# Optimization experiments

Hardware: AMD Instinct MI355X
Metric: run time of the kernel (lower is better)

## Reference

```python
import jax, jax.numpy as jnp
import numpy as np

B, S, D_MODEL, D_FORWARD, HEAD = 4, 2048, 1024, 1024, 16
D_K = D_FORWARD // HEAD


def setup_inputs() -> dict:
    key = jax.random.key(0)
    ks = jax.random.split(key, 6)
    scale = 1.0 / np.sqrt(D_MODEL)
    x = jax.random.normal(ks[0], (B, S, D_MODEL), dtype=jnp.float32)
    # per-head projection weights, PyTorch Linear layout [out, in] stacked over heads
    Wq = jax.random.normal(ks[1], (HEAD, D_K, D_MODEL), dtype=jnp.float32) * scale
    Wk = jax.random.normal(ks[2], (HEAD, D_K, D_MODEL), dtype=jnp.float32) * scale
    Wv = jax.random.normal(ks[3], (HEAD, D_K, D_MODEL), dtype=jnp.float32) * scale
    Wo = jax.random.normal(ks[4], (D_MODEL, D_FORWARD), dtype=jnp.float32) * (1.0 / np.sqrt(D_FORWARD))
    bo = jax.random.normal(ks[5], (D_MODEL,), dtype=jnp.float32) * 0.01
    return {"x": x, "Wq": Wq, "Wk": Wk, "Wv": Wv, "Wo": Wo, "bo": bo}


def reference(x, Wq, Wk, Wv, Wo, bo):
    d_k = Wq.shape[1]
    # fused per-head projections: q,k,v are [B, H, S, d_k]
    q = jnp.einsum("bsm,hkm->bhsk", x, Wq)
    k = jnp.einsum("bsm,hkm->bhsk", x, Wk)
    v = jnp.einsum("bsm,hkm->bhsk", x, Wv)
    # raw scores [B, H, S, S]
    scores = jnp.einsum("bhqd,bhkd->bhqk", q, k)
    # custom zero-value mask: entries that are exactly 0 get -1e9
    scores = jnp.where(scores != 0, scores, jnp.float32(-1e9))
    # NOTE: original divides by scale_factor = d_k**-0.5, i.e. multiplies by sqrt(d_k)
    att = jax.nn.softmax(scores * jnp.sqrt(jnp.float32(d_k)), axis=-1)
    z = jnp.einsum("bhqk,bhkd->bhqd", att, v)  # [B, H, S, d_k]
    n_batch, h, s, _ = z.shape
    z = jnp.transpose(z, (0, 2, 1, 3)).reshape(n_batch, s, h * d_k)  # [B, S, d_forward]
    return z @ Wo.T + bo
```

## Files before the change

kernel.cpp:

```cpp
#include <hip/hip_runtime.h>
#include <stdint.h>

typedef __attribute__((ext_vector_type(4))) float f32x4;
typedef __attribute__((ext_vector_type(8))) _Float16 half8;
typedef __attribute__((ext_vector_type(4))) unsigned int u32x4;
typedef __attribute__((ext_vector_type(2))) unsigned int u32x2;

#define MFMA_F16(a, b, c) __builtin_amdgcn_mfma_f32_16x16x32_f16(a, b, c, 0, 0, 0)

#define GLD16(gp, lp)                                                          \
  __builtin_amdgcn_global_load_lds(                                            \
      (const __attribute__((address_space(1))) void*)(gp),                     \
      (__attribute__((address_space(3))) void*)(lp), 16, 0, 0)

__device__ __forceinline__ short f2h(float f) {
  union { _Float16 h; short s; } v;
  v.h = (_Float16)f;
  return v.s;
}
__device__ __forceinline__ float exp2_hw(float x) {
  float r;
  asm("v_exp_f32 %0, %1" : "=v"(r) : "v"(x));
  return r;
}
__device__ __forceinline__ uint32_t pkhf(float lo, float hi) {
  uint32_t r;
  asm("v_cvt_pkrtz_f16_f32 %0, %1, %2" : "=v"(r) : "v"(lo), "v"(hi));
  return r;
}

__global__ __launch_bounds__(256) void cast4_f16(const float* __restrict__ src,
                                                 short* __restrict__ d, int n4) {
  int i = blockIdx.x * 256 + threadIdx.x;
  if (i < n4) {
    f32x4 v = *reinterpret_cast<const f32x4*>(src + (size_t)i * 4);
    u32x2 o;
    o[0] = pkhf(v[0], v[1]);
    o[1] = pkhf(v[2], v[3]);
    *reinterpret_cast<u32x2*>(d + (size_t)i * 4) = o;
  }
}

__global__ __launch_bounds__(256) void gemm_proj(
    const short* __restrict__ Xf, const short* __restrict__ Wf,
    short* __restrict__ Qf, short* __restrict__ Kf, short* __restrict__ Vt) {
  __shared__ short sA[128 * 32], sB[128 * 32];
  const int tid = threadIdx.x, lane = tid & 63, w = tid >> 6;
  const int wr = w >> 1, wc = w & 1;
  const int g = lane >> 4, c = lane & 15;
  const int m0 = blockIdx.y * 128, n0 = blockIdx.x * 128;

  f32x4 acc[4][4];
#pragma unroll
  for (int i = 0; i < 4; i++)
#pragma unroll
    for (int j = 0; j < 4; j++) acc[i][j] = (f32x4){0.f, 0.f, 0.f, 0.f};

  const int swG = (g ^ ((c >> 1) & 3)) * 8;

  for (int ks = 0; ks < 32; ks++) {
    const int k0 = ks * 32;
    __syncthreads();
#pragma unroll
    for (int i = 0; i < 2; i++) {
      const int chunk = i * 256 + w * 64 + lane;
      const int row = chunk >> 2;
      const int colg = (chunk & 3) ^ ((row >> 1) & 3);
      const size_t aoff = (size_t)(m0 + row) * 1024 + k0 + colg * 8;
      const size_t boff = (size_t)(n0 + row) * 1024 + k0 + colg * 8;
      const int ldsoff = chunk * 16;
      GLD16(Xf + aoff, (char*)sA + ldsoff);
      GLD16(Wf + boff, (char*)sB + ldsoff);
    }
    asm volatile("s_waitcnt vmcnt(0)" ::: "memory");
    __syncthreads();

    half8 a[4], b8[4];
#pragma unroll
    for (int i = 0; i < 4; i++) {
      a[i] = *(const half8*)&sA[(wr * 64 + i * 16 + c) * 32 + swG];
      b8[i] = *(const half8*)&sB[(wc * 64 + i * 16 + c) * 32 + swG];
    }
#pragma unroll
    for (int i = 0; i < 4; i++)
#pragma unroll
      for (int j = 0; j < 4; j++) acc[i][j] = MFMA_F16(a[i], b8[j], acc[i][j]);
  }

  const int section = n0 >> 10;
#pragma unroll
  for (int i = 0; i < 4; i++)
#pragma unroll
    for (int j = 0; j < 4; j++)
#pragma unroll
      for (int r = 0; r < 4; r++) {
        const float v = acc[i][j][r];
        const int m = m0 + wr * 64 + i * 16 + g * 4 + r;
        const int n = n0 + wc * 64 + j * 16 + c;
        const int b = m >> 11, s = m & 2047;
        const int nn = n & 1023;
        const int hh = nn >> 6, d = nn & 63;
        if (section == 0) {
          const size_t off = ((size_t)(b * 16 + hh) * 2048 + s) * 64 + d;
          Qf[off] = f2h(v * 11.5415603271f);
        } else if (section == 1) {
          const size_t off = ((size_t)(b * 16 + hh) * 2048 + s) * 64 + d;
          Kf[off] = f2h(v);
        } else {
          Vt[((size_t)(b * 16 + hh) * 64 + d) * 2048 + s] = f2h(v);
        }
      }
}

__global__ __launch_bounds__(256) void attn_kernel(
    const short* __restrict__ Qf, const short* __restrict__ Kf,
    const short* __restrict__ Vt, short* __restrict__ Z) {
  __shared__ short sK[2][64 * 64];
  __shared__ short sV[2][64 * 64];
  const int tid = threadIdx.x, lane = tid & 63, w = tid >> 6;
  const int g = lane >> 4, c = lane & 15;
  const int L = blockIdx.x;
  const int wid = (L & 7) * 256 + (L >> 3);
  const int qblk = wid & 31, bh = wid >> 5;
  const int b = bh >> 4, h = bh & 15;
  const size_t base = (size_t)bh * (2048 * 64);

  half8 qf[2];
  {
    const int qrow = qblk * 64 + w * 16 + c;
#pragma unroll
    for (int cc = 0; cc < 2; cc++) {
      const size_t off = base + (size_t)qrow * 64 + cc * 32 + g * 8;
      qf[cc] = *(const half8*)(Qf + off);
    }
  }

  f32x4 zacc[4];
  float m_run = -INFINITY, l_part = 0.f;
#pragma unroll
  for (int dt = 0; dt < 4; dt++) zacc[dt] = (f32x4){0.f, 0.f, 0.f, 0.f};

  const int sw0 = ((0 * 4 + g) ^ (c & 7)) * 8;
  const int sw1 = ((1 * 4 + g) ^ (c & 7)) * 8;

  const int ch0 = tid, ch1 = tid + 256;
  const int kr0 = ch0 >> 3, kc0 = (ch0 & 7) ^ (kr0 & 7);
  const int kr1 = ch1 >> 3, kc1 = (ch1 & 7) ^ (kr1 & 7);
  const int kofs0 = kr0 * 64 + kc0 * 8, kofs1 = kr1 * 64 + kc1 * 8;
  const int vofs0 = kr0 * 2048 + kc0 * 8, vofs1 = kr1 * 2048 + kc1 * 8;
  const int ldo0 = ch0 * 16, ldo1 = ch1 * 16;

  auto stage = [&](int buf, int kt) {
    const size_t kb = base + (size_t)kt * 4096;
    const size_t vb = base + (size_t)kt * 64;
    GLD16(Kf + kb + kofs0, (char*)&sK[buf][0] + ldo0);
    GLD16(Kf + kb + kofs1, (char*)&sK[buf][0] + ldo1);
    GLD16(Vt + vb + vofs0, (char*)&sV[buf][0] + ldo0);
    GLD16(Vt + vb + vofs1, (char*)&sV[buf][0] + ldo1);
  };

  const int srcl = ((g & 1) << 5) + c;

  auto compute = [&](int buf) {
    f32x4 sacc[4];
#pragma unroll
    for (int t = 0; t < 4; t++) sacc[t] = (f32x4){0.f, 0.f, 0.f, 0.f};
    __builtin_amdgcn_s_setprio(1);
#pragma unroll
    for (int cc = 0; cc < 2; cc++) {
      const int sw = cc ? sw1 : sw0;
#pragma unroll
      for (int t = 0; t < 4; t++) {
        const int kr = (t * 16 + c) * 64 + sw;
        half8 k8 = *(const half8*)&sK[buf][kr];
        sacc[t] = MFMA_F16(k8, qf[cc], sacc[t]);
      }
    }
    __builtin_amdgcn_s_setprio(0);

    float p[16];
#pragma unroll
    for (int t = 0; t < 4; t++)
#pragma unroll
      for (int r = 0; r < 4; r++) p[t * 4 + r] = sacc[t][r];
    float m01 = fmaxf(fmaxf(fmaxf(p[0], p[1]), fmaxf(p[2], p[3])),
                      fmaxf(fmaxf(p[4], p[5]), fmaxf(p[6], p[7])));
    float m23 = fmaxf(fmaxf(fmaxf(p[8], p[9]), fmaxf(p[10], p[11])),
                      fmaxf(fmaxf(p[12], p[13]), fmaxf(p[14], p[15])));
    float mx = fmaxf(m01, m23);
    mx = fmaxf(mx, __shfl_xor(mx, 16));
    mx = fmaxf(mx, __shfl_xor(mx, 32));
    if (__any(mx - m_run > 8.0f)) {
      const float mnew = fmaxf(m_run, mx);
      const float sc = exp2_hw(m_run - mnew);
      m_run = mnew;
      l_part *= sc;
#pragma unroll
      for (int dt = 0; dt < 4; dt++)
#pragma unroll
        for (int r = 0; r < 4; r++) zacc[dt][r] *= sc;
    }
#pragma unroll
    for (int i = 0; i < 16; i++) p[i] = exp2_hw(p[i] - m_run);
    l_part += (((p[0] + p[1]) + (p[2] + p[3])) + ((p[4] + p[5]) + (p[6] + p[7]))) +
              (((p[8] + p[9]) + (p[10] + p[11])) +
               ((p[12] + p[13]) + (p[14] + p[15])));

    union { u32x4 u; half8 s; } pf0, pf1;
    {
      const uint32_t wA0 = pkhf(p[0], p[1]), wA1 = pkhf(p[2], p[3]);
      const uint32_t wB0 = pkhf(p[4], p[5]), wB1 = pkhf(p[6], p[7]);
      const uint32_t a0 = __shfl(wA0, srcl), a1 = __shfl(wA1, srcl);
      const uint32_t b0 = __shfl(wB0, srcl), b1 = __shfl(wB1, srcl);
      const uint32_t a2 = __shfl(wA0, srcl + 16), a3 = __shfl(wA1, srcl + 16);
      const uint32_t b2 = __shfl(wB0, srcl + 16), b3 = __shfl(wB1, srcl + 16);
      pf0.u[0] = (g < 2) ? a0 : b0;
      pf0.u[1] = (g < 2) ? a1 : b1;
      pf0.u[2] = (g < 2) ? a2 : b2;
      pf0.u[3] = (g < 2) ? a3 : b3;
    }
    {
      const uint32_t wA0 = pkhf(p[8], p[9]), wA1 = pkhf(p[10], p[11]);
      const uint32_t wB0 = pkhf(p[12], p[13]), wB1 = pkhf(p[14], p[15]);
      const uint32_t a0 = __shfl(wA0, srcl), a1 = __shfl(wA1, srcl);
      const uint32_t b0 = __shfl(wB0, srcl), b1 = __shfl(wB1, srcl);
      const uint32_t a2 = __shfl(wA0, srcl + 16), a3 = __shfl(wA1, srcl + 16);
      const uint32_t b2 = __shfl(wB0, srcl + 16), b3 = __shfl(wB1, srcl + 16);
      pf1.u[0] = (g < 2) ? a0 : b0;
      pf1.u[1] = (g < 2) ? a1 : b1;
      pf1.u[2] = (g < 2) ? a2 : b2;
      pf1.u[3] = (g < 2) ? a3 : b3;
    }

    __builtin_amdgcn_s_setprio(1);
#pragma unroll
    for (int dt = 0; dt < 4; dt++) {
      const int vr = (dt * 16 + c) * 64;
      half8 vb0 = *(const half8*)&sV[buf][vr + sw0];
      half8 vb1 = *(const half8*)&sV[buf][vr + sw1];
      zacc[dt] = MFMA_F16(vb0, pf0.s, zacc[dt]);
      zacc[dt] = MFMA_F16(vb1, pf1.s, zacc[dt]);
    }
    __builtin_amdgcn_s_setprio(0);
  };

  stage(0, 0);
  asm volatile("s_waitcnt vmcnt(0)" ::: "memory");
  __builtin_amdgcn_s_barrier();

#pragma unroll 1
  for (int t2 = 0; t2 < 16; t2++) {
    {
      stage(1, 2 * t2 + 1);
      compute(0);
      asm volatile("s_waitcnt vmcnt(0) lgkmcnt(0)" ::: "memory");
      __builtin_amdgcn_s_barrier();
    }
    {
      const int nxt = 2 * t2 + 2;
      stage(0, nxt < 32 ? nxt : 31);
      compute(1);
      asm volatile("s_waitcnt vmcnt(0) lgkmcnt(0)" ::: "memory");
      __builtin_amdgcn_s_barrier();
    }
  }

  float rs = l_part;
  rs += __shfl_xor(rs, 16);
  rs += __shfl_xor(rs, 32);
  const float inv = rs > 0.f ? 1.0f / rs : 0.f;
  const int qg = qblk * 64 + w * 16 + c;
#pragma unroll
  for (int dt = 0; dt < 4; dt++) {
    u32x2 zw;
    zw[0] = pkhf(zacc[dt][0] * inv, zacc[dt][1] * inv);
    zw[1] = pkhf(zacc[dt][2] * inv, zacc[dt][3] * inv);
    *reinterpret_cast<u32x2*>(
        &Z[(size_t)(b * 2048 + qg) * 1024 + h * 64 + dt * 16 + g * 4]) = zw;
  }
}

__global__ __launch_bounds__(256) void gemm_out(
    const short* __restrict__ Zb, const short* __restrict__ Wof,
    const float* __restrict__ bo, float* __restrict__ out) {
  __shared__ short sA[128 * 32], sB[128 * 32];
  const int tid = threadIdx.x, lane = tid & 63, w = tid >> 6;
  const int wr = w >> 1, wc = w & 1;
  const int g = lane >> 4, c = lane & 15;
  const int m0 = blockIdx.y * 128, n0 = blockIdx.x * 128;

  f32x4 acc[4][4];
#pragma unroll
  for (int i = 0; i < 4; i++)
#pragma unroll
    for (int j = 0; j < 4; j++) acc[i][j] = (f32x4){0.f, 0.f, 0.f, 0.f};

  const int swG = (g ^ ((c >> 1) & 3)) * 8;

  for (int ks = 0; ks < 32; ks++) {
    const int k0 = ks * 32;
    __syncthreads();
#pragma unroll
    for (int i = 0; i < 2; i++) {
      const int chunk = i * 256 + w * 64 + lane;
      const int row = chunk >> 2;
      const int colg = (chunk & 3) ^ ((row >> 1) & 3);
      const size_t aoff = (size_t)(m0 + row) * 1024 + k0 + colg * 8;
      const size_t boff = (size_t)(n0 + row) * 1024 + k0 + colg * 8;
      const int ldsoff = chunk * 16;
      GLD16(Zb + aoff, (char*)sA + ldsoff);
      GLD16(Wof + boff, (char*)sB + ldsoff);
    }
    asm volatile("s_waitcnt vmcnt(0)" ::: "memory");
    __syncthreads();

    half8 a[4], b8[4];
#pragma unroll
    for (int i = 0; i < 4; i++) {
      a[i] = *(const half8*)&sA[(wr * 64 + i * 16 + c) * 32 + swG];
      b8[i] = *(const half8*)&sB[(wc * 64 + i * 16 + c) * 32 + swG];
    }
#pragma unroll
    for (int i = 0; i < 4; i++)
#pragma unroll
      for (int j = 0; j < 4; j++) acc[i][j] = MFMA_F16(a[i], b8[j], acc[i][j]);
  }

#pragma unroll
  for (int i = 0; i < 4; i++)
#pragma unroll
    for (int j = 0; j < 4; j++)
#pragma unroll
      for (int r = 0; r < 4; r++) {
        const int m = m0 + wr * 64 + i * 16 + g * 4 + r;
        const int n = n0 + wc * 64 + j * 16 + c;
        out[(size_t)m * 1024 + n] = acc[i][j][r] + bo[n];
      }
}

extern "C" void kernel_launch(void* const* d_in, const int* in_sizes, int n_in,
                              void* d_out, int out_size, void* d_ws, size_t ws_size,
                              hipStream_t stream) {
  const float* x  = (const float*)d_in[0];
  const float* Wq = (const float*)d_in[1];
  const float* Wk = (const float*)d_in[2];
  const float* Wv = (const float*)d_in[3];
  const float* Wo = (const float*)d_in[4];
  const float* bo = (const float*)d_in[5];
  float* out = (float*)d_out;

  const size_t NX = 8388608;
  const size_t NW = 1048576;
  const size_t NQ = 8388608;

  char* p = (char*)d_ws;
  auto take = [&](size_t bytes) -> char* {
    char* r = p;
    p += (bytes + 255) & ~(size_t)255;
    return r;
  };
  short* Xf  = (short*)take(NX * 2);
  short* Wf  = (short*)take(3 * NW * 2);
  short* Wof = (short*)take(NW * 2);
  short* Qf  = (short*)take(NQ * 2);
  short* Kf  = (short*)take(NQ * 2);
  short* Vt  = (short*)take(NQ * 2);
  short* Zb  = (short*)take(NQ * 2);

  cast4_f16<<<dim3((int)(NX / 1024)), 256, 0, stream>>>(x, Xf, (int)(NX / 4));
  cast4_f16<<<dim3((int)(NW / 1024)), 256, 0, stream>>>(Wq, Wf, (int)(NW / 4));
  cast4_f16<<<dim3((int)(NW / 1024)), 256, 0, stream>>>(Wk, Wf + NW, (int)(NW / 4));
  cast4_f16<<<dim3((int)(NW / 1024)), 256, 0, stream>>>(Wv, Wf + 2 * NW, (int)(NW / 4));
  cast4_f16<<<dim3((int)(NW / 1024)), 256, 0, stream>>>(Wo, Wof, (int)(NW / 4));

  gemm_proj<<<dim3(24, 64), 256, 0, stream>>>(Xf, Wf, Qf, Kf, Vt);
  attn_kernel<<<dim3(2048), 256, 0, stream>>>(Qf, Kf, Vt, Zb);
  gemm_out<<<dim3(8, 64), 256, 0, stream>>>(Zb, Wof, bo, out);
}
```

Before: 264.4 us.

## Process two query sub-tiles per wave in attention to reuse K/V fragments

Each attention block now handles 128 query rows instead of 64, with each wave computing two 16-row sub-tiles that share the same K and V LDS fragment loads, halving the grid and the total K/V traffic. The row-sum of probabilities is now accumulated via an MFMA against a ones vector instead of scalar adds plus cross-lane shuffles. This raises register pressure (launch bounds set to 4 blocks) and halves the number of blocks, which may reduce occupancy and load balance.

```diff
diff --git a/kernel.cpp b/kernel.cpp
--- a/kernel.cpp
+++ b/kernel.cpp
@@ -112,7 +112,7 @@
       }
 }
 
-__global__ __launch_bounds__(256) void attn_kernel(
+__global__ __launch_bounds__(256, 4) void attn_kernel(
     const short* __restrict__ Qf, const short* __restrict__ Kf,
     const short* __restrict__ Vt, short* __restrict__ Z) {
   __shared__ short sK[2][64 * 64];
@@ -120,25 +120,37 @@
   const int tid = threadIdx.x, lane = tid & 63, w = tid >> 6;
   const int g = lane >> 4, c = lane & 15;
   const int L = blockIdx.x;
-  const int wid = (L & 7) * 256 + (L >> 3);
-  const int qblk = wid & 31, bh = wid >> 5;
+  const int wid = (L & 7) * 128 + (L >> 3);
+  const int qblk = wid & 15, bh = wid >> 4;
   const int b = bh >> 4, h = bh & 15;
   const size_t base = (size_t)bh * (2048 * 64);
 
-  half8 qf[2];
+  half8 qf[2][2];
   {
-    const int qrow = qblk * 64 + w * 16 + c;
-#pragma unroll
-    for (int cc = 0; cc < 2; cc++) {
-      const size_t off = base + (size_t)qrow * 64 + cc * 32 + g * 8;
-      qf[cc] = *(const half8*)(Qf + off);
-    }
-  }
-
-  f32x4 zacc[4];
-  float m_run = -INFINITY, l_part = 0.f;
-#pragma unroll
-  for (int dt = 0; dt < 4; dt++) zacc[dt] = (f32x4){0.f, 0.f, 0.f, 0.f};
+    const int qrow = qblk * 128 + w * 32 + c;
+#pragma unroll
+    for (int qi = 0; qi < 2; qi++)
+#pragma unroll
+      for (int cc = 0; cc < 2; cc++) {
+        const size_t off =
+            base + (size_t)(qrow + qi * 16) * 64 + cc * 32 + g * 8;
+        qf[qi][cc] = *(const half8*)(Qf + off);
+      }
+  }
+
+  f32x4 zacc[2][4];
+  f32x4 lacc[2];
+  float m_run[2] = {-INFINITY, -INFINITY};
+#pragma unroll
+  for (int qi = 0; qi < 2; qi++) {
+    lacc[qi] = (f32x4){0.f, 0.f, 0.f, 0.f};
+#pragma unroll
+    for (int dt = 0; dt < 4; dt++) zacc[qi][dt] = (f32x4){0.f, 0.f, 0.f, 0.f};
+  }
+
+  half8 ones;
+#pragma unroll
+  for (int i = 0; i < 8; i++) ones[i] = (_Float16)1.0f;
 
   const int sw0 = ((0 * 4 + g) ^ (c & 7)) * 8;
   const int sw1 = ((1 * 4 + g) ^ (c & 7)) * 8;
@@ -162,9 +174,11 @@
   const int srcl = ((g & 1) << 5) + c;
 
   auto compute = [&](int buf) {
-    f32x4 sacc[4];
-#pragma unroll
-    for (int t = 0; t < 4; t++) sacc[t] = (f32x4){0.f, 0.f, 0.f, 0.f};
+    f32x4 sacc[2][4];
+#pragma unroll
+    for (int qi = 0; qi < 2; qi++)
+#pragma unroll
+      for (int t = 0; t < 4; t++) sacc[qi][t] = (f32x4){0.f, 0.f, 0.f, 0.f};
     __builtin_amdgcn_s_setprio(1);
 #pragma unroll
     for (int cc = 0; cc < 2; cc++) {
@@ -173,73 +187,124 @@
       for (int t = 0; t < 4; t++) {
         const int kr = (t * 16 + c) * 64 + sw;
         half8 k8 = *(const half8*)&sK[buf][kr];
-        sacc[t] = MFMA_F16(k8, qf[cc], sacc[t]);
+        sacc[0][t] = MFMA_F16(k8, qf[0][cc], sacc[0][t]);
+        sacc[1][t] = MFMA_F16(k8, qf[1][cc], sacc[1][t]);
       }
     }
     __builtin_amdgcn_s_setprio(0);
 
-    float p[16];
+    float p0[16], p1[16];
 #pragma unroll
     for (int t = 0; t < 4; t++)
 #pragma unroll
-      for (int r = 0; r < 4; r++) p[t * 4 + r] = sacc[t][r];
-    float m01 = fmaxf(fmaxf(fmaxf(p[0], p[1]), fmaxf(p[2], p[3])),
-                      fmaxf(fmaxf(p[4], p[5]), fmaxf(p[6], p[7])));
-    float m23 = fmaxf(fmaxf(fmaxf(p[8], p[9]), fmaxf(p[10], p[11])),
-                      fmaxf(fmaxf(p[12], p[13]), fmaxf(p[14], p[15])));
-    float mx = fmaxf(m01, m23);
-    mx = fmaxf(mx, __shfl_xor(mx, 16));
-    mx = fmaxf(mx, __shfl_xor(mx, 32));
-    if (__any(mx - m_run > 8.0f)) {
-      const float mnew = fmaxf(m_run, mx);
-      const float sc = exp2_hw(m_run - mnew);
-      m_run = mnew;
-      l_part *= sc;
-#pragma unroll
-      for (int dt = 0; dt < 4; dt++)
-#pragma unroll
-        for (int r = 0; r < 4; r++) zacc[dt][r] *= sc;
-    }
-#pragma unroll
-    for (int i = 0; i < 16; i++) p[i] = exp2_hw(p[i] - m_run);
-    l_part += (((p[0] + p[1]) + (p[2] + p[3])) + ((p[4] + p[5]) + (p[6] + p[7]))) +
-              (((p[8] + p[9]) + (p[10] + p[11])) +
-               ((p[12] + p[13]) + (p[14] + p[15])));
-
-    union { u32x4 u; half8 s; } pf0, pf1;
-    {
-      const uint32_t wA0 = pkhf(p[0], p[1]), wA1 = pkhf(p[2], p[3]);
-      const uint32_t wB0 = pkhf(p[4], p[5]), wB1 = pkhf(p[6], p[7]);
+      for (int r = 0; r < 4; r++) {
+        p0[t * 4 + r] = sacc[0][t][r];
+        p1[t * 4 + r] = sacc[1][t][r];
+      }
+    float mx0, mx1;
+    {
+      float a = fmaxf(fmaxf(fmaxf(p0[0], p0[1]), fmaxf(p0[2], p0[3])),
+                      fmaxf(fmaxf(p0[4], p0[5]), fmaxf(p0[6], p0[7])));
+      float bq = fmaxf(fmaxf(fmaxf(p0[8], p0[9]), fmaxf(p0[10], p0[11])),
+                       fmaxf(fmaxf(p0[12], p0[13]), fmaxf(p0[14], p0[15])));
+      mx0 = fmaxf(a, bq);
+      mx0 = fmaxf(mx0, __shfl_xor(mx0, 16));
+      mx0 = fmaxf(mx0, __shfl_xor(mx0, 32));
+    }
+    {
+      float a = fmaxf(fmaxf(fmaxf(p1[0], p1[1]), fmaxf(p1[2], p1[3])),
+                      fmaxf(fmaxf(p1[4], p1[5]), fmaxf(p1[6], p1[7])));
+      float bq = fmaxf(fmaxf(fmaxf(p1[8], p1[9]), fmaxf(p1[10], p1[11])),
+                       fmaxf(fmaxf(p1[12], p1[13]), fmaxf(p1[14], p1[15])));
+      mx1 = fmaxf(a, bq);
+      mx1 = fmaxf(mx1, __shfl_xor(mx1, 16));
+      mx1 = fmaxf(mx1, __shfl_xor(mx1, 32));
+    }
+    const float growmax = fmaxf(mx0 - m_run[0], mx1 - m_run[1]);
+    if (__any(growmax > 8.0f)) {
+#pragma unroll
+      for (int qi = 0; qi < 2; qi++) {
+        const float mnew = fmaxf(m_run[qi], qi ? mx1 : mx0);
+        const float sc = exp2_hw(m_run[qi] - mnew);
+        m_run[qi] = mnew;
+#pragma unroll
+        for (int r = 0; r < 4; r++) lacc[qi][r] *= sc;
+#pragma unroll
+        for (int dt = 0; dt < 4; dt++)
+#pragma unroll
+          for (int r = 0; r < 4; r++) zacc[qi][dt][r] *= sc;
+      }
+    }
+#pragma unroll
+    for (int i = 0; i < 16; i++) {
+      p0[i] = exp2_hw(p0[i] - m_run[0]);
+      p1[i] = exp2_hw(p1[i] - m_run[1]);
+    }
+
+    union { u32x4 u; half8 s; } pfa0, pfa1, pfb0, pfb1;
+    {
+      const uint32_t wA0 = pkhf(p0[0], p0[1]), wA1 = pkhf(p0[2], p0[3]);
+      const uint32_t wB0 = pkhf(p0[4], p0[5]), wB1 = pkhf(p0[6], p0[7]);
       const uint32_t a0 = __shfl(wA0, srcl), a1 = __shfl(wA1, srcl);
       const uint32_t b0 = __shfl(wB0, srcl), b1 = __shfl(wB1, srcl);
       const uint32_t a2 = __shfl(wA0, srcl + 16), a3 = __shfl(wA1, srcl + 16);
       const uint32_t b2 = __shfl(wB0, srcl + 16), b3 = __shfl(wB1, srcl + 16);
-      pf0.u[0] = (g < 2) ? a0 : b0;
-      pf0.u[1] = (g < 2) ? a1 : b1;
-      pf0.u[2] = (g < 2) ? a2 : b2;
-      pf0.u[3] = (g < 2) ? a3 : b3;
-    }
-    {
-      const uint32_t wA0 = pkhf(p[8], p[9]), wA1 = pkhf(p[10], p[11]);
-      const uint32_t wB0 = pkhf(p[12], p[13]), wB1 = pkhf(p[14], p[15]);
+      pfa0.u[0] = (g < 2) ? a0 : b0;
+      pfa0.u[1] = (g < 2) ? a1 : b1;
+      pfa0.u[2] = (g < 2) ? a2 : b2;
+      pfa0.u[3] = (g < 2) ? a3 : b3;
+    }
+    {
+      const uint32_t wA0 = pkhf(p0[8], p0[9]), wA1 = pkhf(p0[10], p0[11]);
+      const uint32_t wB0 = pkhf(p0[12], p0[13]), wB1 = pkhf(p0[14], p0[15]);
       const uint32_t a0 = __shfl(wA0, srcl), a1 = __shfl(wA1, srcl);
       const uint32_t b0 = __shfl(wB0, srcl), b1 = __shfl(wB1, srcl);
       const uint32_t a2 = __shfl(wA0, srcl + 16), a3 = __shfl(wA1, srcl + 16);
       const uint32_t b2 = __shfl(wB0, srcl + 16), b3 = __shfl(wB1, srcl + 16);
-      pf1.u[0] = (g < 2) ? a0 : b0;
-      pf1.u[1] = (g < 2) ? a1 : b1;
-      pf1.u[2] = (g < 2) ? a2 : b2;
-      pf1.u[3] = (g < 2) ? a3 : b3;
+      pfa1.u[0] = (g < 2) ? a0 : b0;
+      pfa1.u[1] = (g < 2) ? a1 : b1;
+      pfa1.u[2] = (g < 2) ? a2 : b2;
+      pfa1.u[3] = (g < 2) ? a3 : b3;
+    }
+    {
+      const uint32_t wA0 = pkhf(p1[0], p1[1]), wA1 = pkhf(p1[2], p1[3]);
+      const uint32_t wB0 = pkhf(p1[4], p1[5]), wB1 = pkhf(p1[6], p1[7]);
+      const uint32_t a0 = __shfl(wA0, srcl), a1 = __shfl(wA1, srcl);
+      const uint32_t b0 = __shfl(wB0, srcl), b1 = __shfl(wB1, srcl);
+      const uint32_t a2 = __shfl(wA0, srcl + 16), a3 = __shfl(wA1, srcl + 16);
+      const uint32_t b2 = __shfl(wB0, srcl + 16), b3 = __shfl(wB1, srcl + 16);
+      pfb0.u[0] = (g < 2) ? a0 : b0;
+      pfb0.u[1] = (g < 2) ? a1 : b1;
+      pfb0.u[2] = (g < 2) ? a2 : b2;
+      pfb0.u[3] = (g < 2) ? a3 : b3;
+    }
+    {
+      const uint32_t wA0 = pkhf(p1[8], p1[9]), wA1 = pkhf(p1[10], p1[11]);
+      const uint32_t wB0 = pkhf(p1[12], p1[13]), wB1 = pkhf(p1[14], p1[15]);
+      const uint32_t a0 = __shfl(wA0, srcl), a1 = __shfl(wA1, srcl);
+      const uint32_t b0 = __shfl(wB0, srcl), b1 = __shfl(wB1, srcl);
+      const uint32_t a2 = __shfl(wA0, srcl + 16), a3 = __shfl(wA1, srcl + 16);
+      const uint32_t b2 = __shfl(wB0, srcl + 16), b3 = __shfl(wB1, srcl + 16);
+      pfb1.u[0] = (g < 2) ? a0 : b0;
+      pfb1.u[1] = (g < 2) ? a1 : b1;
+      pfb1.u[2] = (g < 2) ? a2 : b2;
+      pfb1.u[3] = (g < 2) ? a3 : b3;
     }
 
     __builtin_amdgcn_s_setprio(1);
+    lacc[0] = MFMA_F16(ones, pfa0.s, lacc[0]);
+    lacc[0] = MFMA_F16(ones, pfa1.s, lacc[0]);
+    lacc[1] = MFMA_F16(ones, pfb0.s, lacc[1]);
+    lacc[1] = MFMA_F16(ones, pfb1.s, lacc[1]);
 #pragma unroll
     for (int dt = 0; dt < 4; dt++) {
       const int vr = (dt * 16 + c) * 64;
       half8 vb0 = *(const half8*)&sV[buf][vr + sw0];
       half8 vb1 = *(const half8*)&sV[buf][vr + sw1];
-      zacc[dt] = MFMA_F16(vb0, pf0.s, zacc[dt]);
-      zacc[dt] = MFMA_F16(vb1, pf1.s, zacc[dt]);
+      zacc[0][dt] = MFMA_F16(vb0, pfa0.s, zacc[0][dt]);
+      zacc[0][dt] = MFMA_F16(vb1, pfa1.s, zacc[0][dt]);
+      zacc[1][dt] = MFMA_F16(vb0, pfb0.s, zacc[1][dt]);
+      zacc[1][dt] = MFMA_F16(vb1, pfb1.s, zacc[1][dt]);
     }
     __builtin_amdgcn_s_setprio(0);
   };
@@ -265,18 +330,20 @@
     }
   }
 
-  float rs = l_part;
-  rs += __shfl_xor(rs, 16);
-  rs += __shfl_xor(rs, 32);
-  const float inv = rs > 0.f ? 1.0f / rs : 0.f;
-  const int qg = qblk * 64 + w * 16 + c;
-#pragma unroll
-  for (int dt = 0; dt < 4; dt++) {
-    u32x2 zw;
-    zw[0] = pkhf(zacc[dt][0] * inv, zacc[dt][1] * inv);
-    zw[1] = pkhf(zacc[dt][2] * inv, zacc[dt][3] * inv);
-    *reinterpret_cast<u32x2*>(
-        &Z[(size_t)(b * 2048 + qg) * 1024 + h * 64 + dt * 16 + g * 4]) = zw;
+  const int qg0 = qblk * 128 + w * 32 + c;
+#pragma unroll
+  for (int qi = 0; qi < 2; qi++) {
+    const float rs = lacc[qi][0];
+    const float inv = rs > 0.f ? 1.0f / rs : 0.f;
+    const int qg = qg0 + qi * 16;
+#pragma unroll
+    for (int dt = 0; dt < 4; dt++) {
+      u32x2 zw;
+      zw[0] = pkhf(zacc[qi][dt][0] * inv, zacc[qi][dt][1] * inv);
+      zw[1] = pkhf(zacc[qi][dt][2] * inv, zacc[qi][dt][3] * inv);
+      *reinterpret_cast<u32x2*>(
+          &Z[(size_t)(b * 2048 + qg) * 1024 + h * 64 + dt * 16 + g * 4]) = zw;
+    }
   }
 }
 
@@ -374,6 +441,6 @@
   cast4_f16<<<dim3((int)(NW / 1024)), 256, 0, stream>>>(Wo, Wof, (int)(NW / 4));
 
   gemm_proj<<<dim3(24, 64), 256, 0, stream>>>(Xf, Wf, Qf, Kf, Vt);
-  attn_kernel<<<dim3(2048), 256, 0, stream>>>(Qf, Kf, Vt, Zb);
+  attn_kernel<<<dim3(1024), 256, 0, stream>>>(Qf, Kf, Vt, Zb);
   gemm_out<<<dim3(8, 64), 256, 0, stream>>>(Zb, Wof, bo, out);
 }
```

Measured after the change: 240.6 us. 9.0% less time.
